# Performance work log

Hardware: AMD Instinct MI355X
Metric: run time of the kernel (lower is better)

## Reference

```python
import jax, jax.numpy as jnp
import numpy as np

N_QUBITS = 12
N_LAYERS = 6
BATCH = 512
DIM = 2 ** N_QUBITS


def _apply_1q(psi, G, wire):
    """Apply a single-qubit gate on `wire` (wire 0 = most significant).
    psi: [B, 2^n] complex. G: [2,2] (shared) or [B,2,2] (batched)."""
    B = psi.shape[0]
    left = 2 ** wire
    psi = psi.reshape(B, left, 2, -1)
    if G.ndim == 2:
        psi = jnp.einsum('ij,bxjy->bxiy', G, psi)
    else:
        psi = jnp.einsum('bij,bxjy->bxiy', G, psi)
    return psi.reshape(B, -1)


def _apply_cnot(psi, c, t):
    """CNOT with control c, target t on [B, 2^n] state."""
    B = psi.shape[0]
    ps = psi.reshape((B,) + (2,) * N_QUBITS)
    ca, ta = c + 1, t + 1
    c0 = jnp.take(ps, 0, axis=ca)
    c1 = jnp.take(ps, 1, axis=ca)
    flip_ax = ta if ta < ca else ta - 1
    c1 = jnp.flip(c1, axis=flip_ax)  # X on target within control=1 block
    ps = jnp.stack([c0, c1], axis=ca)
    return ps.reshape(B, -1)


def _circuit(x, weights):
    B = x.shape[0]
    psi = jnp.zeros((B, DIM), jnp.complex64).at[:, 0].set(1.0)

    # AngleEmbedding: RY(x_w) on each wire (batched gate matrices)
    h = 0.5 * x
    c, s = jnp.cos(h).astype(jnp.complex64), jnp.sin(h).astype(jnp.complex64)
    for w in range(N_QUBITS):
        G = jnp.stack([jnp.stack([c[:, w], -s[:, w]], -1),
                       jnp.stack([s[:, w], c[:, w]], -1)], -2)  # [B,2,2]
        psi = _apply_1q(psi, G, w)

    # StronglyEntanglingLayers: Rot(phi,theta,omega) per wire, then ring of CNOTs
    for l in range(N_LAYERS):
        phi, theta, omega = weights[l, :, 0], weights[l, :, 1], weights[l, :, 2]
        ct = jnp.cos(0.5 * theta).astype(jnp.complex64)
        st = jnp.sin(0.5 * theta).astype(jnp.complex64)
        ep = jnp.exp(-0.5j * (phi + omega).astype(jnp.complex64))
        em = jnp.exp(0.5j * (phi - omega).astype(jnp.complex64))
        # Rot = RZ(omega) RY(theta) RZ(phi)
        m00 = ep * ct
        m01 = -em * st
        m10 = jnp.conj(em) * st
        m11 = jnp.conj(ep) * ct
        for w in range(N_QUBITS):
            G = jnp.array([[m00[w], m01[w]], [m10[w], m11[w]]], jnp.complex64)
            psi = _apply_1q(psi, G, w)
        r = l % (N_QUBITS - 1) + 1
        for w in range(N_QUBITS):
            psi = _apply_cnot(psi, w, (w + r) % N_QUBITS)

    # <Z_w> for every wire
    probs = psi.real ** 2 + psi.imag ** 2  # [B, 2^n]
    exps = []
    for w in range(N_QUBITS):
        p = probs.reshape(B, 2 ** w, 2, -1)
        exps.append(p[:, :, 0, :].sum((1, 2)) - p[:, :, 1, :].sum((1, 2)))
    return jnp.stack(exps, -1)  # [B, n_qubits]


def setup_inputs() -> dict:
    key = jax.random.key(0)
    k1, k2, k3, k4 = jax.random.split(key, 4)
    x = jax.random.uniform(k1, (BATCH, N_QUBITS), jnp.float32, -np.pi, np.pi)
    weights = jax.random.uniform(k2, (N_LAYERS, N_QUBITS, 3), jnp.float32, 0.0, 2.0 * np.pi)
    W = jax.random.normal(k3, (1, N_QUBITS), jnp.float32) * 0.3
    b = jax.random.normal(k4, (1,), jnp.float32) * 0.01
    return {"x": x, "weights": weights, "W": W, "b": b}


def reference(x, weights, W, b):
    z = _circuit(x, weights)              # [B, n_qubits]
    y = z @ W.T + b                       # [B, 1]
    return y.squeeze(-1)                  # [B]
```

## Files before the change

### kernel.cpp

```cpp
#include <hip/hip_runtime.h>
#include <stdint.h>

#define NQ 12
#define DIM 4096
#define NLAYERS 6
#define TPB 256

typedef float v2f __attribute__((ext_vector_type(2)));

struct Pass_t {
    uint32_t WT[8];
    uint32_t WL[8];
    uint32_t RT[8];
    uint32_t RL[16];
    bool r64;
};
struct CK_t {
    Pass_t PS1, PS2, PS3;
    Pass_t P1[NLAYERS];
    uint32_t frow[NQ];
};

constexpr uint32_t S1f(uint32_t k){ return ((k&7u)<<3) | ((k>>3)&7u) | (k & 0xFC0u); }
constexpr uint32_t S2f(uint32_t k){ return ((k&7u)<<6) | (k & 0x38u) | ((k>>6)&7u) | (k & 0xE00u); }
constexpr uint32_t S3f(uint32_t k){ return ((k&7u)<<9) | (k & 0x1F8u) | ((k>>9)&7u); }

constexpr uint32_t ech_reduce(const uint32_t* v, int n, uint32_t x){
    bool ch = true;
    while (ch) {
        ch = false;
        for (int i = 0; i < n; i++)
            if (v[i] && (x ^ v[i]) < x) { x ^= v[i]; ch = true; }
    }
    return x;
}

constexpr Pass_t build_pass(const uint32_t* Mc) {
    Pass_t P{};
    bool r64 = (Mc[3] == 8u);
    for (int j = 0; j < 12; j++) if (j != 3 && (Mc[j] & 8u)) r64 = false;
    P.r64 = r64;

    uint32_t rows[12]{};
    rows[0] = 8u;
    int nr = 1;
    uint32_t full[12]{}; int nf = 0; full[nf++] = 8u;
    uint32_t We[4]{};  int nw = 0;
    uint32_t Re[5]{};  int nre = 0;
    const int rpn = r64 ? 4 : 5;
    if (!r64) {
        uint32_t p0 = 0;
        for (int j = 0; j < rpn; j++)
            p0 |= (uint32_t)(__builtin_popcount(8u & Mc[4 + j]) & 1) << j;
        uint32_t r = ech_reduce(Re, nre, p0);
        if (r) Re[nre++] = r;
    }
    for (int slot = 0; slot < 4; slot++) {
        uint32_t chosen = 0;
        for (int relax = 0; relax < 3 && !chosen; relax++) {
            for (uint32_t m = 1; m < 4096u && !chosen; m++) {
                if (m & 8u) continue;
                uint32_t wp = (m >> 4) & 15u;
                uint32_t wr = ech_reduce(We, nw, wp);
                if (relax < 2 && !wr) continue;
                uint32_t rp = 0;
                for (int j = 0; j < rpn; j++)
                    rp |= (uint32_t)(__builtin_popcount(m & Mc[4 + j]) & 1) << j;
                uint32_t rr = ech_reduce(Re, nre, rp);
                if (relax < 1 && !rr) continue;
                uint32_t fr = ech_reduce(full, nf, m);
                if (!fr) continue;
                chosen = m; full[nf++] = fr;
                if (wr && nw < 4) We[nw++] = wr;
                if (rr && nre < 5) Re[nre++] = rr;
            }
        }
        rows[nr++] = chosen;
    }
    for (int slot = 5; slot < 12; slot++) {
        for (uint32_t m = 1; m < 4096u; m++) {
            if (m & 8u) continue;
            uint32_t fr = ech_reduce(full, nf, m);
            if (fr) { rows[nr++] = m; full[nf++] = fr; break; }
        }
    }
    uint32_t col[12]{}, lmc[12]{};
    for (int j = 0; j < 12; j++) {
        uint32_t c = 0;
        for (int i = 0; i < 12; i++) c |= (uint32_t)((rows[i] >> j) & 1u) << i;
        col[j] = c;
    }
    for (int j = 0; j < 12; j++) {
        uint32_t a = 0, mc = Mc[j];
        for (int q = 0; q < 12; q++) if ((mc >> q) & 1u) a ^= col[q];
        lmc[j] = a;
    }
    for (int j = 0; j < 8; j++) { P.WT[j] = col[4 + j]; P.RT[j] = lmc[4 + j]; }
    for (int j = 0; j < 8; j++) {
        uint32_t a = 0;
        for (int q = 0; q < 3; q++) if ((j >> q) & 1) a ^= col[q];
        P.WL[j] = a;
    }
    for (int l = 0; l < 16; l++) {
        uint32_t a = 0;
        for (int q = 0; q < 4; q++) if ((l >> q) & 1) a ^= lmc[q];
        P.RL[l] = a;
    }
    return P;
}

constexpr CK_t build_ck() {
    CK_t ck{};
    uint32_t Acols[NLAYERS][NQ]{}, Aicol5[NQ]{};
    for (int l = 0; l < NLAYERS; l++) {
        int r = l % (NQ - 1) + 1;
        for (int q = 0; q < NQ; q++) {
            uint32_t v = 1u << q;
            for (int w = NQ - 1; w >= 0; w--) {
                int pc = NQ - 1 - w, pt = NQ - 1 - ((w + r) % NQ);
                v ^= ((v >> pc) & 1u) << pt;
            }
            Acols[l][q] = v;
            if (l == NLAYERS - 1) {
                uint32_t u = 1u << q;
                for (int w = 0; w < NQ; w++) {
                    int pc = NQ - 1 - w, pt = NQ - 1 - ((w + r) % NQ);
                    u ^= ((u >> pc) & 1u) << pt;
                }
                Aicol5[q] = u;
            }
        }
    }
    uint32_t Mc[12]{};
    for (int j = 0; j < 12; j++) Mc[j] = S1f(1u << j);
    ck.PS1 = build_pass(Mc);
    for (int j = 0; j < 12; j++) Mc[j] = S2f(1u << j);
    ck.PS2 = build_pass(Mc);
    for (int j = 0; j < 12; j++) Mc[j] = S3f(1u << j);
    ck.PS3 = build_pass(Mc);
    for (int l = 1; l < NLAYERS; l++) {
        for (int j = 0; j < 12; j++) Mc[j] = S3f(S2f(S1f(Acols[l - 1][j])));
        ck.P1[l] = build_pass(Mc);
    }
    uint32_t Mcol[NQ]{};
    for (int j = 0; j < NQ; j++) {
        uint32_t pj = S1f(S2f(S3f(1u << j)));
        uint32_t M = 0;
        for (int m = 0; m < NQ; m++) if ((pj >> m) & 1u) M ^= Aicol5[m];
        Mcol[j] = M;
    }
    for (int p = 0; p < NQ; p++) {
        uint32_t s = 0;
        for (int j = 0; j < NQ; j++) s |= ((Mcol[j] >> p) & 1u) << j;
        ck.frow[p] = s;
    }
    return ck;
}
constexpr CK_t CK = build_ck();

template<int KIND, int L, int PAR>
__device__ __forceinline__ void do_pass(v2f (&PRE)[8], v2f (&PIM)[8],
                                        float* lds, int tid) {
    constexpr Pass_t P = (KIND == 1) ? CK.P1[L]
                       : (KIND == 2) ? CK.PS1
                       : (KIND == 3) ? CK.PS2 : CK.PS3;
    float* buf = lds + PAR * (2 * DIM);
    uint32_t comb = 0;
    #pragma unroll
    for (int j = 0; j < 8; j++) {
        uint32_t pk = P.WT[j] | (P.RT[j] << 16);
        comb ^= (uint32_t)(-(int)((tid >> j) & 1)) & pk;
    }
    uint32_t wb = comb & 0xFFFFu, rb = comb >> 16;
    v2f* bre = (v2f*)buf;
    v2f* bim = (v2f*)(buf + DIM);
    #pragma unroll
    for (int j = 0; j < 8; j++) {
        uint32_t s = (wb ^ P.WL[j]) >> 1;
        bre[s] = PRE[j];
        bim[s] = PIM[j];
    }
    __syncthreads();
    if constexpr (P.r64) {
        #pragma unroll
        for (int j = 0; j < 8; j++) {
            uint32_t s = (rb ^ P.RL[j]) >> 1;
            PRE[j] = bre[s];
            PIM[j] = bim[s];
        }
    } else {
        #pragma unroll
        for (int j = 0; j < 8; j++) {
            uint32_t s0 = rb ^ P.RL[j], s1 = rb ^ P.RL[j | 8];
            v2f re, im;
            re.x = buf[s0];        re.y = buf[s1];
            im.x = buf[DIM + s0];  im.y = buf[DIM + s1];
            PRE[j] = re;
            PIM[j] = im;
        }
    }
}

template<int L, int W, int Q>
__device__ __forceinline__ void reg_gate(v2f (&PRE)[8], v2f (&PIM)[8],
                                         const float4* smat) {
    float4 m = smat[L * NQ + W];
    v2f bx = {m.x, m.x}, by = {m.y, m.y}, bz = {m.z, m.z}, bw = {m.w, m.w};
    #pragma unroll
    for (int j = 0; j < 8; j++) {
        if (j & (1 << Q)) continue;
        int j2 = j | (1 << Q);
        v2f re0 = PRE[j], im0 = PIM[j], re1 = PRE[j2], im1 = PIM[j2];
        PRE[j]  = __builtin_elementwise_fma(bx, re0,
                  __builtin_elementwise_fma(by, -im0,
                  __builtin_elementwise_fma(bz, re1, -bw * im1)));
        PIM[j]  = __builtin_elementwise_fma(bx, im0,
                  __builtin_elementwise_fma(by, re0,
                  __builtin_elementwise_fma(bz, im1, bw * re1)));
        PRE[j2] = __builtin_elementwise_fma(bx, re1,
                  __builtin_elementwise_fma(by, im1,
                  __builtin_elementwise_fma(bz, -re0, -bw * im0)));
        PIM[j2] = __builtin_elementwise_fma(bx, im1,
                  __builtin_elementwise_fma(by, -re1,
                  __builtin_elementwise_fma(bz, -im0, bw * re0)));
    }
}

template<int L>
__device__ __forceinline__ void do_layer(v2f (&PRE)[8], v2f (&PIM)[8],
                                         const float4* smat, float* lds, int tid) {
    if constexpr (L > 0)
        do_pass<1, L, 1>(PRE, PIM, lds, tid);
    reg_gate<L, 11, 0>(PRE, PIM, smat);
    reg_gate<L, 10, 1>(PRE, PIM, smat);
    reg_gate<L,  9, 2>(PRE, PIM, smat);
    do_pass<2, L, 0>(PRE, PIM, lds, tid);
    reg_gate<L, 8, 0>(PRE, PIM, smat);
    reg_gate<L, 7, 1>(PRE, PIM, smat);
    reg_gate<L, 6, 2>(PRE, PIM, smat);
    do_pass<3, L, 1>(PRE, PIM, lds, tid);
    reg_gate<L, 5, 0>(PRE, PIM, smat);
    reg_gate<L, 4, 1>(PRE, PIM, smat);
    reg_gate<L, 3, 2>(PRE, PIM, smat);
    do_pass<4, L, 0>(PRE, PIM, lds, tid);
    reg_gate<L, 2, 0>(PRE, PIM, smat);
    reg_gate<L, 1, 1>(PRE, PIM, smat);
    reg_gate<L, 0, 2>(PRE, PIM, smat);
}

__global__ __launch_bounds__(TPB) void qsim_kernel(
    const float* __restrict__ x,
    const float* __restrict__ weights,
    const float* __restrict__ Wp,
    const float* __restrict__ bptr,
    float* __restrict__ out)
{
    __shared__ float  lds[2 * 2 * DIM];
    __shared__ float4 smat[NLAYERS * NQ];
    __shared__ float  scs[NQ], sss[NQ];
    __shared__ float  red[4];

    const int tid = threadIdx.x;
    const int b   = blockIdx.x;

    if (tid < NQ) {
        float s_, c_;
        sincosf(0.5f * x[b * NQ + tid], &s_, &c_);
        scs[tid] = c_; sss[tid] = s_;
    }
    if (tid < NLAYERS * NQ) {
        float phi   = weights[tid * 3 + 0];
        float theta = weights[tid * 3 + 1];
        float omega = weights[tid * 3 + 2];
        float st, ct; sincosf(0.5f * theta, &st, &ct);
        float sp, cp; sincosf(0.5f * (phi + omega), &sp, &cp);
        float sm, cm; sincosf(0.5f * (phi - omega), &sm, &cm);
        smat[tid] = make_float4(cp * ct, -sp * ct, -cm * st, -sm * st);
    }
    __syncthreads();

    float base = 1.0f;
    #pragma unroll
    for (int j = 0; j < 8; j++) {
        int w = 7 - j;
        base *= ((tid >> j) & 1) ? sss[w] : scs[w];
    }
    v2f PRE[8], PIM[8];
    float c8 = scs[8], s8 = sss[8];
    #pragma unroll
    for (int j = 0; j < 8; j++) {
        float a = base;
        #pragma unroll
        for (int p = 0; p < 3; p++) {
            int w = NQ - 1 - p;
            a *= ((j >> p) & 1) ? sss[w] : scs[w];
        }
        PRE[j].x = a * c8;  PRE[j].y = a * s8;
        PIM[j].x = 0.0f;    PIM[j].y = 0.0f;
    }

    do_layer<0>(PRE, PIM, smat, lds, tid);
    do_layer<1>(PRE, PIM, smat, lds, tid);
    do_layer<2>(PRE, PIM, smat, lds, tid);
    do_layer<3>(PRE, PIM, smat, lds, tid);
    do_layer<4>(PRE, PIM, smat, lds, tid);
    do_layer<5>(PRE, PIM, smat, lds, tid);

    const float bv = bptr[0];
    float wbT[NQ];
    #pragma unroll
    for (int p = 0; p < NQ; p++) {
        uint32_t row = CK.frow[p];
        int tp = __popc(tid & (int)(row >> 4)) & 1;
        float Wv = Wp[NQ - 1 - p];
        wbT[p] = tp ? -Wv : Wv;
    }
    v2f acc2 = {0.0f, 0.0f};
    #pragma unroll
    for (int j = 0; j < 8; j++) {
        float cx = bv, cy = bv;
        #pragma unroll
        for (int p = 0; p < NQ; p++) {
            uint32_t row = CK.frow[p];
            float s = (__popc(j & (int)(row & 7u)) & 1) ? -wbT[p] : wbT[p];
            cx += s;
            cy += (row & 8u) ? -s : s;
        }
        v2f c = {cx, cy};
        acc2 += (PRE[j] * PRE[j] + PIM[j] * PIM[j]) * c;
    }
    float acc = acc2.x + acc2.y;
    #pragma unroll
    for (int off = 32; off > 0; off >>= 1)
        acc += __shfl_down(acc, off, 64);
    if ((tid & 63) == 0) red[tid >> 6] = acc;
    __syncthreads();
    if (tid == 0) out[b] = red[0] + red[1] + red[2] + red[3];
}

extern "C" void kernel_launch(void* const* d_in, const int* in_sizes, int n_in,
                              void* d_out, int out_size, void* d_ws, size_t ws_size,
                              hipStream_t stream) {
    const float* x       = (const float*)d_in[0];
    const float* weights = (const float*)d_in[1];
    const float* W       = (const float*)d_in[2];
    const float* bptr    = (const float*)d_in[3];
    qsim_kernel<<<512, TPB, 0, stream>>>(x, weights, W, bptr, (float*)d_out);
}
```

Measured before the change: 91.80 us.

## Make S1/S2 transposes wave-local and roll layer loop to cut block barriers

Builds 10-bit pass tables for the S1 and S2 permutations so their exchanges stay within each wavefront's own LDS region, keyed by the two high thread bits. Those passes now use an lgkmcnt wait instead of __syncthreads, leaving block barriers only for the S3 and rebase passes. The six layers become a runtime loop with rebase tables read from constant memory, which shrinks code size but adds runtime indexing. This relies on wave-synchronous LDS ordering within a 64-lane wavefront, and S3 gains an extra leading barrier to protect the shared buffer.

```diff
diff --git a/kernel.cpp b/kernel.cpp
--- a/kernel.cpp
+++ b/kernel.cpp
@@ -15,8 +15,16 @@
     uint32_t RL[16];
     bool r64;
 };
+struct Pass10_t {
+    uint32_t WT[6];
+    uint32_t WL[8];
+    uint32_t RT[6];
+    uint32_t RL[16];
+    bool r64;
+};
 struct CK_t {
-    Pass_t PS1, PS2, PS3;
+    Pass10_t PS1, PS2;
+    Pass_t PS3;
     Pass_t P1[NLAYERS];
     uint32_t frow[NQ];
 };
@@ -40,7 +48,6 @@
     bool r64 = (Mc[3] == 8u);
     for (int j = 0; j < 12; j++) if (j != 3 && (Mc[j] & 8u)) r64 = false;
     P.r64 = r64;
-
     uint32_t rows[12]{};
     rows[0] = 8u;
     int nr = 1;
@@ -77,11 +84,11 @@
         }
         rows[nr++] = chosen;
     }
-    for (int slot = 5; slot < 12; slot++) {
+    for (int slot = nr; slot < 12; slot++) {
         for (uint32_t m = 1; m < 4096u; m++) {
             if (m & 8u) continue;
             uint32_t fr = ech_reduce(full, nf, m);
-            if (fr) { rows[nr++] = m; full[nf++] = fr; break; }
+            if (fr) { rows[slot] = m; full[nf++] = fr; break; }
         }
     }
     uint32_t col[12]{}, lmc[12]{};
@@ -96,6 +103,79 @@
         lmc[j] = a;
     }
     for (int j = 0; j < 8; j++) { P.WT[j] = col[4 + j]; P.RT[j] = lmc[4 + j]; }
+    for (int j = 0; j < 8; j++) {
+        uint32_t a = 0;
+        for (int q = 0; q < 3; q++) if ((j >> q) & 1) a ^= col[q];
+        P.WL[j] = a;
+    }
+    for (int l = 0; l < 16; l++) {
+        uint32_t a = 0;
+        for (int q = 0; q < 4; q++) if ((l >> q) & 1) a ^= lmc[q];
+        P.RL[l] = a;
+    }
+    return P;
+}
+
+constexpr Pass10_t build_pass10(const uint32_t* Mc) {
+    Pass10_t P{};
+    bool r64 = (Mc[3] == 8u);
+    for (int j = 0; j < 10; j++) if (j != 3 && (Mc[j] & 8u)) r64 = false;
+    P.r64 = r64;
+    uint32_t rows[10]{};
+    rows[0] = 8u;
+    int nr = 1;
+    uint32_t full[10]{}; int nf = 0; full[nf++] = 8u;
+    uint32_t We[4]{};  int nw = 0;
+    uint32_t Re[5]{};  int nre = 0;
+    const int rpn = r64 ? 4 : 5;
+    if (!r64) {
+        uint32_t p0 = 0;
+        for (int j = 0; j < rpn; j++)
+            p0 |= (uint32_t)(__builtin_popcount(8u & Mc[4 + j]) & 1) << j;
+        uint32_t r = ech_reduce(Re, nre, p0);
+        if (r) Re[nre++] = r;
+    }
+    for (int slot = 0; slot < 4; slot++) {
+        uint32_t chosen = 0;
+        for (int relax = 0; relax < 3 && !chosen; relax++) {
+            for (uint32_t m = 1; m < 1024u && !chosen; m++) {
+                if (m & 8u) continue;
+                uint32_t wp = (m >> 4) & 15u;
+                uint32_t wr = ech_reduce(We, nw, wp);
+                if (relax < 2 && !wr) continue;
+                uint32_t rp = 0;
+                for (int j = 0; j < rpn; j++)
+                    rp |= (uint32_t)(__builtin_popcount(m & Mc[4 + j]) & 1) << j;
+                uint32_t rr = ech_reduce(Re, nre, rp);
+                if (relax < 1 && !rr) continue;
+                uint32_t fr = ech_reduce(full, nf, m);
+                if (!fr) continue;
+                chosen = m; full[nf++] = fr;
+                if (wr && nw < 4) We[nw++] = wr;
+                if (rr && nre < 5) Re[nre++] = rr;
+            }
+        }
+        rows[nr++] = chosen;
+    }
+    for (int slot = nr; slot < 10; slot++) {
+        for (uint32_t m = 1; m < 1024u; m++) {
+            if (m & 8u) continue;
+            uint32_t fr = ech_reduce(full, nf, m);
+            if (fr) { rows[slot] = m; full[nf++] = fr; break; }
+        }
+    }
+    uint32_t col[10]{}, lmc[10]{};
+    for (int j = 0; j < 10; j++) {
+        uint32_t c = 0;
+        for (int i = 0; i < 10; i++) c |= (uint32_t)((rows[i] >> j) & 1u) << i;
+        col[j] = c;
+    }
+    for (int j = 0; j < 10; j++) {
+        uint32_t a = 0, mc = Mc[j];
+        for (int q = 0; q < 10; q++) if ((mc >> q) & 1u) a ^= col[q];
+        lmc[j] = a;
+    }
+    for (int j = 0; j < 6; j++) { P.WT[j] = col[4 + j]; P.RT[j] = lmc[4 + j]; }
     for (int j = 0; j < 8; j++) {
         uint32_t a = 0;
         for (int q = 0; q < 3; q++) if ((j >> q) & 1) a ^= col[q];
@@ -131,11 +211,12 @@
             }
         }
     }
+    uint32_t Mc10[10]{};
+    for (int j = 0; j < 10; j++) Mc10[j] = S1f(1u << j);
+    ck.PS1 = build_pass10(Mc10);
+    for (int j = 0; j < 10; j++) Mc10[j] = S2f(1u << j);
+    ck.PS2 = build_pass10(Mc10);
     uint32_t Mc[12]{};
-    for (int j = 0; j < 12; j++) Mc[j] = S1f(1u << j);
-    ck.PS1 = build_pass(Mc);
-    for (int j = 0; j < 12; j++) Mc[j] = S2f(1u << j);
-    ck.PS2 = build_pass(Mc);
     for (int j = 0; j < 12; j++) Mc[j] = S3f(1u << j);
     ck.PS3 = build_pass(Mc);
     for (int l = 1; l < NLAYERS; l++) {
@@ -157,54 +238,11 @@
     return ck;
 }
 constexpr CK_t CK = build_ck();
-
-template<int KIND, int L, int PAR>
-__device__ __forceinline__ void do_pass(v2f (&PRE)[8], v2f (&PIM)[8],
-                                        float* lds, int tid) {
-    constexpr Pass_t P = (KIND == 1) ? CK.P1[L]
-                       : (KIND == 2) ? CK.PS1
-                       : (KIND == 3) ? CK.PS2 : CK.PS3;
-    float* buf = lds + PAR * (2 * DIM);
-    uint32_t comb = 0;
-    #pragma unroll
-    for (int j = 0; j < 8; j++) {
-        uint32_t pk = P.WT[j] | (P.RT[j] << 16);
-        comb ^= (uint32_t)(-(int)((tid >> j) & 1)) & pk;
-    }
-    uint32_t wb = comb & 0xFFFFu, rb = comb >> 16;
-    v2f* bre = (v2f*)buf;
-    v2f* bim = (v2f*)(buf + DIM);
-    #pragma unroll
-    for (int j = 0; j < 8; j++) {
-        uint32_t s = (wb ^ P.WL[j]) >> 1;
-        bre[s] = PRE[j];
-        bim[s] = PIM[j];
-    }
-    __syncthreads();
-    if constexpr (P.r64) {
-        #pragma unroll
-        for (int j = 0; j < 8; j++) {
-            uint32_t s = (rb ^ P.RL[j]) >> 1;
-            PRE[j] = bre[s];
-            PIM[j] = bim[s];
-        }
-    } else {
-        #pragma unroll
-        for (int j = 0; j < 8; j++) {
-            uint32_t s0 = rb ^ P.RL[j], s1 = rb ^ P.RL[j | 8];
-            v2f re, im;
-            re.x = buf[s0];        re.y = buf[s1];
-            im.x = buf[DIM + s0];  im.y = buf[DIM + s1];
-            PRE[j] = re;
-            PIM[j] = im;
-        }
-    }
-}
-
-template<int L, int W, int Q>
-__device__ __forceinline__ void reg_gate(v2f (&PRE)[8], v2f (&PIM)[8],
-                                         const float4* smat) {
-    float4 m = smat[L * NQ + W];
+static_assert(CK.PS2.r64, "S2 must fix the pack bit (b64 reads)");
+static_assert(CK.PS3.r64, "S3 must fix the pack bit (b64 reads)");
+
+template<int Q>
+__device__ __forceinline__ void gate_q(v2f (&PRE)[8], v2f (&PIM)[8], float4 m) {
     v2f bx = {m.x, m.x}, by = {m.y, m.y}, bz = {m.z, m.z}, bw = {m.w, m.w};
     #pragma unroll
     for (int j = 0; j < 8; j++) {
@@ -226,26 +264,97 @@
     }
 }
 
-template<int L>
-__device__ __forceinline__ void do_layer(v2f (&PRE)[8], v2f (&PIM)[8],
-                                         const float4* smat, float* lds, int tid) {
-    if constexpr (L > 0)
-        do_pass<1, L, 1>(PRE, PIM, lds, tid);
-    reg_gate<L, 11, 0>(PRE, PIM, smat);
-    reg_gate<L, 10, 1>(PRE, PIM, smat);
-    reg_gate<L,  9, 2>(PRE, PIM, smat);
-    do_pass<2, L, 0>(PRE, PIM, lds, tid);
-    reg_gate<L, 8, 0>(PRE, PIM, smat);
-    reg_gate<L, 7, 1>(PRE, PIM, smat);
-    reg_gate<L, 6, 2>(PRE, PIM, smat);
-    do_pass<3, L, 1>(PRE, PIM, lds, tid);
-    reg_gate<L, 5, 0>(PRE, PIM, smat);
-    reg_gate<L, 4, 1>(PRE, PIM, smat);
-    reg_gate<L, 3, 2>(PRE, PIM, smat);
-    do_pass<4, L, 0>(PRE, PIM, lds, tid);
-    reg_gate<L, 2, 0>(PRE, PIM, smat);
-    reg_gate<L, 1, 1>(PRE, PIM, smat);
-    reg_gate<L, 0, 2>(PRE, PIM, smat);
+__device__ __forceinline__ void gate3(v2f (&PRE)[8], v2f (&PIM)[8],
+                                      float4 g0, float4 g1, float4 g2) {
+    gate_q<0>(PRE, PIM, g0);
+    gate_q<1>(PRE, PIM, g1);
+    gate_q<2>(PRE, PIM, g2);
+}
+
+__device__ __forceinline__ void s1_pass(v2f (&PRE)[8], v2f (&PIM)[8],
+                                        float* buf, uint32_t wb, uint32_t rb) {
+    constexpr Pass10_t P = CK.PS1;
+    v2f* bre = (v2f*)buf;
+    v2f* bim = (v2f*)(buf + DIM);
+    #pragma unroll
+    for (int j = 0; j < 8; j++) {
+        uint32_t s = (wb ^ P.WL[j]) >> 1;
+        bre[s] = PRE[j]; bim[s] = PIM[j];
+    }
+    __asm__ volatile("s_waitcnt lgkmcnt(0)" ::: "memory");
+    #pragma unroll
+    for (int j = 0; j < 8; j++) {
+        uint32_t s0 = rb ^ P.RL[j], s1 = rb ^ P.RL[j | 8];
+        v2f re, im;
+        re.x = buf[s0];       re.y = buf[s1];
+        im.x = buf[DIM + s0]; im.y = buf[DIM + s1];
+        PRE[j] = re; PIM[j] = im;
+    }
+}
+
+__device__ __forceinline__ void s2_pass(v2f (&PRE)[8], v2f (&PIM)[8],
+                                        float* buf, uint32_t wb, uint32_t rb) {
+    constexpr Pass10_t P = CK.PS2;
+    v2f* bre = (v2f*)buf;
+    v2f* bim = (v2f*)(buf + DIM);
+    #pragma unroll
+    for (int j = 0; j < 8; j++) {
+        uint32_t s = (wb ^ P.WL[j]) >> 1;
+        bre[s] = PRE[j]; bim[s] = PIM[j];
+    }
+    __asm__ volatile("s_waitcnt lgkmcnt(0)" ::: "memory");
+    #pragma unroll
+    for (int j = 0; j < 8; j++) {
+        uint32_t s = (rb ^ P.RL[j]) >> 1;
+        PRE[j] = bre[s]; PIM[j] = bim[s];
+    }
+}
+
+__device__ __forceinline__ void s3_pass(v2f (&PRE)[8], v2f (&PIM)[8],
+                                        float* buf, uint32_t wb, uint32_t rb) {
+    constexpr Pass_t P = CK.PS3;
+    v2f* bre = (v2f*)buf;
+    v2f* bim = (v2f*)(buf + DIM);
+    __syncthreads();
+    #pragma unroll
+    for (int j = 0; j < 8; j++) {
+        uint32_t s = (wb ^ P.WL[j]) >> 1;
+        bre[s] = PRE[j]; bim[s] = PIM[j];
+    }
+    __syncthreads();
+    #pragma unroll
+    for (int j = 0; j < 8; j++) {
+        uint32_t s = (rb ^ P.RL[j]) >> 1;
+        PRE[j] = bre[s]; PIM[j] = bim[s];
+    }
+}
+
+__device__ __forceinline__ void rebase_pass(v2f (&PRE)[8], v2f (&PIM)[8],
+                                            float* buf, int tid, int l) {
+    const Pass_t& P = CK.P1[l];
+    uint32_t wb = 0, rb = 0;
+    #pragma unroll
+    for (int j = 0; j < 8; j++) {
+        uint32_t sel = (uint32_t)(-(int)((tid >> j) & 1));
+        wb ^= sel & P.WT[j];
+        rb ^= sel & P.RT[j];
+    }
+    v2f* bre = (v2f*)buf;
+    v2f* bim = (v2f*)(buf + DIM);
+    #pragma unroll
+    for (int j = 0; j < 8; j++) {
+        uint32_t s = (wb ^ P.WL[j]) >> 1;
+        bre[s] = PRE[j]; bim[s] = PIM[j];
+    }
+    __syncthreads();
+    #pragma unroll
+    for (int j = 0; j < 8; j++) {
+        uint32_t s0 = rb ^ P.RL[j], s1 = rb ^ P.RL[j | 8];
+        v2f re, im;
+        re.x = buf[s0];       re.y = buf[s1];
+        im.x = buf[DIM + s0]; im.y = buf[DIM + s1];
+        PRE[j] = re; PIM[j] = im;
+    }
 }
 
 __global__ __launch_bounds__(TPB) void qsim_kernel(
@@ -299,12 +408,41 @@
         PIM[j].x = 0.0f;    PIM[j].y = 0.0f;
     }
 
-    do_layer<0>(PRE, PIM, smat, lds, tid);
-    do_layer<1>(PRE, PIM, smat, lds, tid);
-    do_layer<2>(PRE, PIM, smat, lds, tid);
-    do_layer<3>(PRE, PIM, smat, lds, tid);
-    do_layer<4>(PRE, PIM, smat, lds, tid);
-    do_layer<5>(PRE, PIM, smat, lds, tid);
+    uint32_t s1wb = 0, s1rb = 0, s2wb = 0, s2rb = 0, s3wb = 0, s3rb = 0;
+    {
+        constexpr Pass10_t Q1 = CK.PS1;
+        constexpr Pass10_t Q2 = CK.PS2;
+        constexpr Pass_t   Q3 = CK.PS3;
+        #pragma unroll
+        for (int j = 0; j < 6; j++) {
+            uint32_t sel = (uint32_t)(-(int)((tid >> j) & 1));
+            s1wb ^= sel & Q1.WT[j]; s1rb ^= sel & Q1.RT[j];
+            s2wb ^= sel & Q2.WT[j]; s2rb ^= sel & Q2.RT[j];
+        }
+        #pragma unroll
+        for (int j = 0; j < 8; j++) {
+            uint32_t sel = (uint32_t)(-(int)((tid >> j) & 1));
+            s3wb ^= sel & Q3.WT[j]; s3rb ^= sel & Q3.RT[j];
+        }
+        uint32_t wvb = (uint32_t)(tid & 0xC0) << 4;
+        s1wb |= wvb; s1rb |= wvb; s2wb |= wvb; s2rb |= wvb;
+    }
+
+    float* bufA = lds;
+    float* bufB = lds + 2 * DIM;
+
+    #pragma clang loop unroll(disable)
+    for (int l = 0; l < NLAYERS; l++) {
+        if (l > 0) rebase_pass(PRE, PIM, bufB, tid, l);
+        const int sb = l * NQ;
+        gate3(PRE, PIM, smat[sb + 11], smat[sb + 10], smat[sb + 9]);
+        s1_pass(PRE, PIM, bufA, s1wb, s1rb);
+        gate3(PRE, PIM, smat[sb + 8], smat[sb + 7], smat[sb + 6]);
+        s2_pass(PRE, PIM, bufA, s2wb, s2rb);
+        gate3(PRE, PIM, smat[sb + 5], smat[sb + 4], smat[sb + 3]);
+        s3_pass(PRE, PIM, bufA, s3wb, s3rb);
+        gate3(PRE, PIM, smat[sb + 2], smat[sb + 1], smat[sb + 0]);
+    }
 
     const float bv = bptr[0];
     float wbT[NQ];
```

After: 91.86 us. No clear change (+0.1%).

## Use wave-local LDS transposes and a packed in-register gate to cut block barriers

Applied to the files above, without the earlier changes.

Redesigns the qubit-to-register mapping so that two of the per-layer permutation passes exchange data only within a 64-lane wave. Those passes use an LDS wait instead of a block-wide barrier. One qubit now lives inside each float2 pair and is handled by a new swizzled packed gate. The LDS exchanges use float4 stores and loads. The layer loop is kept rolled, with runtime-indexed rebase tables. It relies on wave-level LDS ordering being correct without __syncthreads, and the rolled loop adds some index-computation overhead.

```diff
diff --git a/kernel.cpp b/kernel.cpp
--- a/kernel.cpp
+++ b/kernel.cpp
@@ -8,22 +8,21 @@
 
 typedef float v2f __attribute__((ext_vector_type(2)));
 
-struct Pass_t {
-    uint32_t WT[8];
-    uint32_t WL[8];
-    uint32_t RT[8];
-    uint32_t RL[16];
-    bool r64;
+struct PB {
+    uint32_t WT[8], WL[8];
+    uint32_t RT[8], RL[8];
+    uint32_t BT[8], BL[16];
 };
 struct CK_t {
-    Pass_t PS1, PS2, PS3;
-    Pass_t P1[NLAYERS];
+    PB PS1, PS2, PS3;
+    PB P1[NLAYERS];
     uint32_t frow[NQ];
 };
 
-constexpr uint32_t S1f(uint32_t k){ return ((k&7u)<<3) | ((k>>3)&7u) | (k & 0xFC0u); }
-constexpr uint32_t S2f(uint32_t k){ return ((k&7u)<<6) | (k & 0x38u) | ((k>>6)&7u) | (k & 0xE00u); }
-constexpr uint32_t S3f(uint32_t k){ return ((k&7u)<<9) | (k & 0x1F8u) | ((k>>9)&7u); }
+constexpr uint32_t S1n(uint32_t k){ return ((k&7u)<<4) | ((k>>4)&7u) | (k & 0xF88u); }
+constexpr uint32_t S2n(uint32_t k){ return ((k&7u)<<7) | ((k>>7)&7u) | (k & 0xC78u); }
+constexpr uint32_t S3n(uint32_t k){ return ((k&3u)<<10) | ((k>>10)&3u) | (k & 0x3FCu); }
+constexpr uint32_t rearr(uint32_t u){ return ((u>>1)<<4) | ((u&1u)<<2); }
 
 constexpr uint32_t ech_reduce(const uint32_t* v, int n, uint32_t x){
     bool ch = true;
@@ -35,76 +34,64 @@
     return x;
 }
 
-constexpr Pass_t build_pass(const uint32_t* Mc) {
-    Pass_t P{};
-    bool r64 = (Mc[3] == 8u);
-    for (int j = 0; j < 12; j++) if (j != 3 && (Mc[j] & 8u)) r64 = false;
-    P.r64 = r64;
-
-    uint32_t rows[12]{};
-    rows[0] = 8u;
-    int nr = 1;
+constexpr PB build_pb(const uint32_t* Mc, int nb) {
+    uint32_t rows[12]{}; rows[0] = 8u; int nr = 1;
     uint32_t full[12]{}; int nf = 0; full[nf++] = 8u;
-    uint32_t We[4]{};  int nw = 0;
-    uint32_t Re[5]{};  int nre = 0;
-    const int rpn = r64 ? 4 : 5;
-    if (!r64) {
-        uint32_t p0 = 0;
-        for (int j = 0; j < rpn; j++)
-            p0 |= (uint32_t)(__builtin_popcount(8u & Mc[4 + j]) & 1) << j;
-        uint32_t r = ech_reduce(Re, nre, p0);
-        if (r) Re[nre++] = r;
-    }
-    for (int slot = 0; slot < 4; slot++) {
+    uint32_t Wsp[3] = {1u<<4, 1u<<5, 1u<<6};
+    uint32_t Rsp[3] = {Mc[4], Mc[5], Mc[6]};
+    uint32_t eW[3]{}, eR[3]{}; int nW = 0, nR = 0;
+    for (int slot = 0; slot < 3; slot++) {
         uint32_t chosen = 0;
         for (int relax = 0; relax < 3 && !chosen; relax++) {
-            for (uint32_t m = 1; m < 4096u && !chosen; m++) {
+            for (uint32_t m = 1; m < (1u << nb) && !chosen; m++) {
                 if (m & 8u) continue;
-                uint32_t wp = (m >> 4) & 15u;
-                uint32_t wr = ech_reduce(We, nw, wp);
+                uint32_t wp = 0, rp = 0;
+                for (int j = 0; j < 3; j++) {
+                    wp |= (uint32_t)(__builtin_popcount(m & Wsp[j]) & 1) << j;
+                    rp |= (uint32_t)(__builtin_popcount(m & Rsp[j]) & 1) << j;
+                }
+                uint32_t wr = ech_reduce(eW, nW, wp);
                 if (relax < 2 && !wr) continue;
-                uint32_t rp = 0;
-                for (int j = 0; j < rpn; j++)
-                    rp |= (uint32_t)(__builtin_popcount(m & Mc[4 + j]) & 1) << j;
-                uint32_t rr = ech_reduce(Re, nre, rp);
+                uint32_t rr = ech_reduce(eR, nR, rp);
                 if (relax < 1 && !rr) continue;
                 uint32_t fr = ech_reduce(full, nf, m);
                 if (!fr) continue;
                 chosen = m; full[nf++] = fr;
-                if (wr && nw < 4) We[nw++] = wr;
-                if (rr && nre < 5) Re[nre++] = rr;
+                if (wr && nW < 3) eW[nW++] = wr;
+                if (rr && nR < 3) eR[nR++] = rr;
             }
         }
         rows[nr++] = chosen;
     }
-    for (int slot = 5; slot < 12; slot++) {
-        for (uint32_t m = 1; m < 4096u; m++) {
+    for (int s = nr; s < nb; s++) {
+        for (uint32_t m = 1; m < (1u << nb); m++) {
             if (m & 8u) continue;
             uint32_t fr = ech_reduce(full, nf, m);
-            if (fr) { rows[nr++] = m; full[nf++] = fr; break; }
+            if (fr) { rows[s] = m; full[nf++] = fr; break; }
         }
     }
     uint32_t col[12]{}, lmc[12]{};
     for (int j = 0; j < 12; j++) {
-        uint32_t c = 0;
-        for (int i = 0; i < 12; i++) c |= (uint32_t)((rows[i] >> j) & 1u) << i;
-        col[j] = c;
+        if (j < nb) {
+            uint32_t c = 0;
+            for (int i = 0; i < nb; i++) c |= (uint32_t)((rows[i] >> j) & 1u) << i;
+            col[j] = c;
+        } else col[j] = 1u << j;
     }
     for (int j = 0; j < 12; j++) {
         uint32_t a = 0, mc = Mc[j];
         for (int q = 0; q < 12; q++) if ((mc >> q) & 1u) a ^= col[q];
         lmc[j] = a;
     }
-    for (int j = 0; j < 8; j++) { P.WT[j] = col[4 + j]; P.RT[j] = lmc[4 + j]; }
-    for (int j = 0; j < 8; j++) {
-        uint32_t a = 0;
-        for (int q = 0; q < 3; q++) if ((j >> q) & 1) a ^= col[q];
-        P.WL[j] = a;
-    }
-    for (int l = 0; l < 16; l++) {
-        uint32_t a = 0;
-        for (int q = 0; q < 4; q++) if ((l >> q) & 1) a ^= lmc[q];
-        P.RL[l] = a;
+    PB P{};
+    for (int j = 0; j < 8; j++) {
+        P.WT[j] = col[4 + j]; P.RT[j] = lmc[4 + j]; P.BT[j] = rearr(lmc[4 + j]);
+    }
+    for (int j = 0; j < 8; j++) {
+        uint32_t a = 0, b = 0;
+        for (int q = 0; q < 3; q++) if ((j >> q) & 1) { a ^= col[q]; b ^= lmc[q]; }
+        P.WL[j] = a; P.RL[j] = b;
+        P.BL[j] = rearr(b); P.BL[8 + j] = rearr(b ^ lmc[3]);
     }
     return P;
 }
@@ -132,19 +119,19 @@
         }
     }
     uint32_t Mc[12]{};
-    for (int j = 0; j < 12; j++) Mc[j] = S1f(1u << j);
-    ck.PS1 = build_pass(Mc);
-    for (int j = 0; j < 12; j++) Mc[j] = S2f(1u << j);
-    ck.PS2 = build_pass(Mc);
-    for (int j = 0; j < 12; j++) Mc[j] = S3f(1u << j);
-    ck.PS3 = build_pass(Mc);
+    for (int j = 0; j < 12; j++) Mc[j] = S1n(1u << j);
+    ck.PS1 = build_pb(Mc, 10);
+    for (int j = 0; j < 12; j++) Mc[j] = S2n(1u << j);
+    ck.PS2 = build_pb(Mc, 10);
+    for (int j = 0; j < 12; j++) Mc[j] = S3n(1u << j);
+    ck.PS3 = build_pb(Mc, 12);
     for (int l = 1; l < NLAYERS; l++) {
-        for (int j = 0; j < 12; j++) Mc[j] = S3f(S2f(S1f(Acols[l - 1][j])));
-        ck.P1[l] = build_pass(Mc);
+        for (int j = 0; j < 12; j++) Mc[j] = S3n(S2n(S1n(Acols[l - 1][j])));
+        ck.P1[l] = build_pb(Mc, 12);
     }
     uint32_t Mcol[NQ]{};
     for (int j = 0; j < NQ; j++) {
-        uint32_t pj = S1f(S2f(S3f(1u << j)));
+        uint32_t pj = S1n(S2n(S3n(1u << j)));
         uint32_t M = 0;
         for (int m = 0; m < NQ; m++) if ((pj >> m) & 1u) M ^= Aicol5[m];
         Mcol[j] = M;
@@ -158,53 +145,8 @@
 }
 constexpr CK_t CK = build_ck();
 
-template<int KIND, int L, int PAR>
-__device__ __forceinline__ void do_pass(v2f (&PRE)[8], v2f (&PIM)[8],
-                                        float* lds, int tid) {
-    constexpr Pass_t P = (KIND == 1) ? CK.P1[L]
-                       : (KIND == 2) ? CK.PS1
-                       : (KIND == 3) ? CK.PS2 : CK.PS3;
-    float* buf = lds + PAR * (2 * DIM);
-    uint32_t comb = 0;
-    #pragma unroll
-    for (int j = 0; j < 8; j++) {
-        uint32_t pk = P.WT[j] | (P.RT[j] << 16);
-        comb ^= (uint32_t)(-(int)((tid >> j) & 1)) & pk;
-    }
-    uint32_t wb = comb & 0xFFFFu, rb = comb >> 16;
-    v2f* bre = (v2f*)buf;
-    v2f* bim = (v2f*)(buf + DIM);
-    #pragma unroll
-    for (int j = 0; j < 8; j++) {
-        uint32_t s = (wb ^ P.WL[j]) >> 1;
-        bre[s] = PRE[j];
-        bim[s] = PIM[j];
-    }
-    __syncthreads();
-    if constexpr (P.r64) {
-        #pragma unroll
-        for (int j = 0; j < 8; j++) {
-            uint32_t s = (rb ^ P.RL[j]) >> 1;
-            PRE[j] = bre[s];
-            PIM[j] = bim[s];
-        }
-    } else {
-        #pragma unroll
-        for (int j = 0; j < 8; j++) {
-            uint32_t s0 = rb ^ P.RL[j], s1 = rb ^ P.RL[j | 8];
-            v2f re, im;
-            re.x = buf[s0];        re.y = buf[s1];
-            im.x = buf[DIM + s0];  im.y = buf[DIM + s1];
-            PRE[j] = re;
-            PIM[j] = im;
-        }
-    }
-}
-
-template<int L, int W, int Q>
-__device__ __forceinline__ void reg_gate(v2f (&PRE)[8], v2f (&PIM)[8],
-                                         const float4* smat) {
-    float4 m = smat[L * NQ + W];
+template<int Q>
+__device__ __forceinline__ void gate_q(v2f (&PRE)[8], v2f (&PIM)[8], float4 m) {
     v2f bx = {m.x, m.x}, by = {m.y, m.y}, bz = {m.z, m.z}, bw = {m.w, m.w};
     #pragma unroll
     for (int j = 0; j < 8; j++) {
@@ -226,26 +168,71 @@
     }
 }
 
-template<int L>
-__device__ __forceinline__ void do_layer(v2f (&PRE)[8], v2f (&PIM)[8],
-                                         const float4* smat, float* lds, int tid) {
-    if constexpr (L > 0)
-        do_pass<1, L, 1>(PRE, PIM, lds, tid);
-    reg_gate<L, 11, 0>(PRE, PIM, smat);
-    reg_gate<L, 10, 1>(PRE, PIM, smat);
-    reg_gate<L,  9, 2>(PRE, PIM, smat);
-    do_pass<2, L, 0>(PRE, PIM, lds, tid);
-    reg_gate<L, 8, 0>(PRE, PIM, smat);
-    reg_gate<L, 7, 1>(PRE, PIM, smat);
-    reg_gate<L, 6, 2>(PRE, PIM, smat);
-    do_pass<3, L, 1>(PRE, PIM, lds, tid);
-    reg_gate<L, 5, 0>(PRE, PIM, smat);
-    reg_gate<L, 4, 1>(PRE, PIM, smat);
-    reg_gate<L, 3, 2>(PRE, PIM, smat);
-    do_pass<4, L, 0>(PRE, PIM, lds, tid);
-    reg_gate<L, 2, 0>(PRE, PIM, smat);
-    reg_gate<L, 1, 1>(PRE, PIM, smat);
-    reg_gate<L, 0, 2>(PRE, PIM, smat);
+__device__ __forceinline__ void pack_gate(v2f (&PRE)[8], v2f (&PIM)[8], float4 m) {
+    v2f d1 = {-m.y, m.y}, d2 = {m.z, -m.z};
+    #pragma unroll
+    for (int j = 0; j < 8; j++) {
+        v2f RE = PRE[j], IM = PIM[j];
+        v2f sR = {RE.y, RE.x}, sI = {IM.y, IM.x};
+        PRE[j] = m.x * RE + d1 * IM + d2 * sR - m.w * sI;
+        PIM[j] = m.x * IM - d1 * RE + d2 * sI + m.w * sR;
+    }
+}
+
+template<int KIND>
+__device__ __forceinline__ void wl_pass(v2f (&PRE)[8], v2f (&PIM)[8],
+                                        char* buf, uint32_t wb, uint32_t rb) {
+    constexpr PB P = (KIND == 1) ? CK.PS1 : CK.PS2;
+    #pragma unroll
+    for (int j = 0; j < 8; j++)
+        *(float4*)(buf + ((wb ^ P.WL[j]) << 3)) =
+            make_float4(PRE[j].x, PRE[j].y, PIM[j].x, PIM[j].y);
+    __asm__ volatile("s_waitcnt lgkmcnt(0)" ::: "memory");
+    #pragma unroll
+    for (int j = 0; j < 8; j++) {
+        float4 v = *(const float4*)(buf + ((rb ^ P.RL[j]) << 3));
+        PRE[j] = v2f{v.x, v.y}; PIM[j] = v2f{v.z, v.w};
+    }
+}
+
+__device__ __forceinline__ void s3_pass(v2f (&PRE)[8], v2f (&PIM)[8],
+                                        char* buf, uint32_t wb, uint32_t rb) {
+    constexpr PB P = CK.PS3;
+    __syncthreads();
+    #pragma unroll
+    for (int j = 0; j < 8; j++)
+        *(float4*)(buf + ((wb ^ P.WL[j]) << 3)) =
+            make_float4(PRE[j].x, PRE[j].y, PIM[j].x, PIM[j].y);
+    __syncthreads();
+    #pragma unroll
+    for (int j = 0; j < 8; j++) {
+        float4 v = *(const float4*)(buf + ((rb ^ P.RL[j]) << 3));
+        PRE[j] = v2f{v.x, v.y}; PIM[j] = v2f{v.z, v.w};
+    }
+}
+
+__device__ __forceinline__ void rebase(v2f (&PRE)[8], v2f (&PIM)[8],
+                                       char* buf, int tid, int l) {
+    const PB& P = CK.P1[l];
+    uint32_t wb = 0, bb = 0;
+    #pragma unroll
+    for (int j = 0; j < 8; j++) {
+        uint32_t sel = (uint32_t)(-(int)((tid >> j) & 1));
+        wb ^= sel & P.WT[j];
+        bb ^= sel & P.BT[j];
+    }
+    #pragma unroll
+    for (int j = 0; j < 8; j++)
+        *(float4*)(buf + ((wb ^ P.WL[j]) << 3)) =
+            make_float4(PRE[j].x, PRE[j].y, PIM[j].x, PIM[j].y);
+    __syncthreads();
+    #pragma unroll
+    for (int j = 0; j < 8; j++) {
+        const float* p0 = (const float*)(buf + (bb ^ P.BL[j]));
+        const float* p1 = (const float*)(buf + (bb ^ P.BL[8 + j]));
+        PRE[j] = v2f{p0[0], p1[0]};
+        PIM[j] = v2f{p0[2], p1[2]};
+    }
 }
 
 __global__ __launch_bounds__(TPB) void qsim_kernel(
@@ -255,7 +242,8 @@
     const float* __restrict__ bptr,
     float* __restrict__ out)
 {
-    __shared__ float  lds[2 * 2 * DIM];
+    __shared__ float4 bufA[DIM / 2];
+    __shared__ float4 bufB[DIM / 2];
     __shared__ float4 smat[NLAYERS * NQ];
     __shared__ float  scs[NQ], sss[NQ];
     __shared__ float  red[4];
@@ -299,12 +287,40 @@
         PIM[j].x = 0.0f;    PIM[j].y = 0.0f;
     }
 
-    do_layer<0>(PRE, PIM, smat, lds, tid);
-    do_layer<1>(PRE, PIM, smat, lds, tid);
-    do_layer<2>(PRE, PIM, smat, lds, tid);
-    do_layer<3>(PRE, PIM, smat, lds, tid);
-    do_layer<4>(PRE, PIM, smat, lds, tid);
-    do_layer<5>(PRE, PIM, smat, lds, tid);
+    uint32_t s1wb = 0, s1rb = 0, s2wb = 0, s2rb = 0, s3wb = 0, s3rb = 0;
+    #pragma unroll
+    for (int j = 0; j < 8; j++) {
+        uint32_t sel = (uint32_t)(-(int)((tid >> j) & 1));
+        s1wb ^= sel & CK.PS1.WT[j]; s1rb ^= sel & CK.PS1.RT[j];
+        s2wb ^= sel & CK.PS2.WT[j]; s2rb ^= sel & CK.PS2.RT[j];
+        s3wb ^= sel & CK.PS3.WT[j]; s3rb ^= sel & CK.PS3.RT[j];
+    }
+
+    char* bA = (char*)bufA;
+    char* bB = (char*)bufB;
+
+    #pragma clang loop unroll(disable)
+    for (int l = 0; l < NLAYERS; l++) {
+        float4 M[12];
+        #pragma unroll
+        for (int w = 0; w < 12; w++) M[w] = smat[l * NQ + w];
+        if (l > 0) rebase(PRE, PIM, bB, tid, l);
+        gate_q<0>(PRE, PIM, M[11]);
+        gate_q<1>(PRE, PIM, M[10]);
+        gate_q<2>(PRE, PIM, M[9]);
+        pack_gate(PRE, PIM, M[8]);
+        wl_pass<1>(PRE, PIM, bA, s1wb, s1rb);
+        gate_q<0>(PRE, PIM, M[7]);
+        gate_q<1>(PRE, PIM, M[6]);
+        gate_q<2>(PRE, PIM, M[5]);
+        wl_pass<2>(PRE, PIM, bA, s2wb, s2rb);
+        gate_q<0>(PRE, PIM, M[4]);
+        gate_q<1>(PRE, PIM, M[3]);
+        gate_q<2>(PRE, PIM, M[2]);
+        s3_pass(PRE, PIM, bA, s3wb, s3rb);
+        gate_q<0>(PRE, PIM, M[1]);
+        gate_q<1>(PRE, PIM, M[0]);
+    }
 
     const float bv = bptr[0];
     float wbT[NQ];
```

Measured after the change: 91.05 us. No clear change (-0.8%).
